# Kernel tuning notes

Measured on AMD Instinct MI355X. Metric: run time of the kernel, lower is better.

The kernel has to match this reference:

```python
import jax, jax.numpy as jnp
import numpy as np

EPS = 1e-8

def setup_inputs() -> dict:
    key = jax.random.key(0)
    ks = jax.random.split(key, 10)
    N, IN, Z, C, H = 8192, 512, 128, 64, 50
    x = jax.random.normal(ks[0], (N, IN), dtype=jnp.float32)
    c = jax.random.randint(ks[1], (N, 1), 0, C, dtype=jnp.int64)
    z = jax.random.normal(ks[2], (N, Z), dtype=jnp.float32)
    # f_x MLP params (Linear(IN,50) -> ReLU -> Linear(50,Z))
    W1 = jax.random.normal(ks[3], (IN, H), dtype=jnp.float32) / np.sqrt(IN)
    b1 = jax.random.normal(ks[4], (H,), dtype=jnp.float32) * 0.01
    W2 = jax.random.normal(ks[5], (H, Z), dtype=jnp.float32) / np.sqrt(H)
    b2 = jax.random.normal(ks[6], (Z,), dtype=jnp.float32) * 0.01
    # f_z Linear(Z,Z)
    Wz = jax.random.normal(ks[7], (Z, Z), dtype=jnp.float32) / np.sqrt(Z)
    bz = jax.random.normal(ks[8], (Z,), dtype=jnp.float32) * 0.01
    # per-category bilinear weights w_s [C,Z,Z] (torch.randn init)
    Ws = jax.random.normal(ks[9], (C, Z, Z), dtype=jnp.float32)
    return {"x": x, "c": c, "z": z, "W1": W1, "b1": b1, "W2": W2, "b2": b2, "Wz": Wz, "bz": bz, "Ws": Ws}

def reference(x, c, z, W1, b1, W2, b2, Wz, bz, Ws):
    cf = c.reshape(-1)                                    # [N]
    fx = jax.nn.relu(x @ W1 + b1) @ W2 + b2               # [N,Z]
    fz = z @ Wz + bz                                      # [N,Z]
    # per-sample bilinear: u[n] = fx[n] @ Ws[c[n]]
    u = jnp.einsum('nd,nde->ne', fx, Ws[cf])              # [N,Z]
    T = jax.nn.softplus(jnp.einsum('ne,ne->n', u, fz))    # [N]
    # neg_T[i] = mean over j with c[j]==c[i] of softplus(fx[i] @ Ws[c[i]] @ fz[j])
    S = jax.nn.softplus(u @ fz.T)                         # [N,N]
    mask = (cf[:, None] == cf[None, :]).astype(S.dtype)   # [N,N]
    neg_T = (S * mask).sum(axis=1) / mask.sum(axis=1)     # [N]
    return jnp.log(T + EPS) - jnp.log(neg_T + EPS)
```

## Files before the change

### kernel.cpp

```cpp
#include <hip/hip_runtime.h>
#include <math.h>

#define N_   8192
#define IN_  512
#define ZD   128
#define CC   64
#define HD   50
#define EPSF 1e-8f

typedef float vf4 __attribute__((ext_vector_type(4)));
typedef __attribute__((ext_vector_type(8))) short bfrag;

#define MFMA16(a, b, c) __builtin_amdgcn_mfma_f32_16x16x32_bf16((a), (b), (c), 0, 0, 0)

__device__ __forceinline__ float softplus_hot(float t) {
    return fmaxf(t, 0.f) + __logf(1.f + __expf(-fabsf(t)));
}
__device__ __forceinline__ float softplus_acc(float t) {
    return fmaxf(t, 0.f) + log1pf(expf(-fabsf(t)));
}
__device__ __forceinline__ unsigned short bf16_rn(float x) {
    unsigned int u = __float_as_uint(x);
    return (unsigned short)((u + 0x7fff + ((u >> 16) & 1)) >> 16);
}
__device__ __forceinline__ float bf16_f(unsigned short h) {
    return __uint_as_float(((unsigned int)h) << 16);
}
__device__ __forceinline__ void split8(const float* v, bfrag& hi, bfrag& lo) {
    #pragma unroll
    for (int e = 0; e < 8; ++e) {
        unsigned short h = bf16_rn(v[e]);
        ((short*)&hi)[e] = (short)h;
        ((short*)&lo)[e] = (short)bf16_rn(v[e] - bf16_f(h));
    }
}

__global__ __launch_bounds__(256) void k_pre(const int* __restrict__ c,
                                             const float* __restrict__ W1,
                                             const float* __restrict__ z,
                                             const float* __restrict__ Wz,
                                             const float* __restrict__ bz,
                                             const float* __restrict__ W2,
                                             const float* __restrict__ Ws,
                                             uint4* __restrict__ W1p,
                                             uint4* __restrict__ W2p,
                                             float* __restrict__ fz,
                                             unsigned short* __restrict__ fz_hi,
                                             unsigned short* __restrict__ Wst_hi,
                                             unsigned short* __restrict__ Wst_lo,
                                             int* __restrict__ counts,
                                             int* __restrict__ offsets,
                                             int* __restrict__ grouped) {
    __shared__ float smem[64 * 129];
    int tid = threadIdx.x;
    int b   = blockIdx.x;
    if (b < CC) {
        __shared__ int hist[CC];
        __shared__ int cursor;
        __shared__ int off_s;
        if (tid < CC) hist[tid] = 0;
        if (tid == 0) cursor = 0;
        __syncthreads();
        for (int i = tid; i < N_; i += 256) atomicAdd(&hist[c[i]], 1);
        __syncthreads();
        if (tid == 0) {
            int off = 0;
            for (int q = 0; q < b; ++q) off += hist[q];
            off_s = off;
            counts[b]  = hist[b];
            offsets[b] = off;
        }
        __syncthreads();
        int off = off_s;
        for (int i = tid; i < N_; i += 256) {
            if (c[i] == b) {
                int p = atomicAdd(&cursor, 1);
                grouped[off + p] = i;
            }
        }
    } else if (b < 80) {
        int unit = (b - 64) * 256 + tid;
        int lane = unit & 63, f = (unit >> 6) & 15, kc = unit >> 10;
        int nt = f >> 2, ks = f & 3;
        int n = nt * 16 + (lane & 15);
        int kbase = kc * 128 + ks * 32 + (lane >> 4) * 8;
        unsigned short hi8[8], lo8[8];
        #pragma unroll
        for (int j = 0; j < 8; ++j) {
            int k = kbase + j;
            float v = (n < HD) ? W1[k * HD + n] : 0.f;
            unsigned short h = bf16_rn(v);
            hi8[j] = h;
            lo8[j] = bf16_rn(v - bf16_f(h));
        }
        W1p[kc * 2048 + f * 64 + lane]        = *(uint4*)hi8;
        W1p[kc * 2048 + 1024 + f * 64 + lane] = *(uint4*)lo8;
    } else if (b < 84) {
        int unit = (b - 80) * 256 + tid;
        int lane = unit & 63, f = unit >> 6;
        int nt = f >> 1, ks = f & 1;
        int n = nt * 16 + (lane & 15);
        int kbase = ks * 32 + (lane >> 4) * 8;
        unsigned short hi8[8], lo8[8];
        #pragma unroll
        for (int j = 0; j < 8; ++j) {
            int k = kbase + j;
            float v = (k < HD) ? W2[k * ZD + n] : 0.f;
            unsigned short h = bf16_rn(v);
            hi8[j] = h;
            lo8[j] = bf16_rn(v - bf16_f(h));
        }
        W2p[f * 64 + lane]        = *(uint4*)hi8;
        W2p[1024 + f * 64 + lane] = *(uint4*)lo8;
    } else if (b < 212) {
        float* sz = smem;
        int row0 = (b - 84) * 64;
        vf4* s4 = (vf4*)sz;
        const vf4* z4 = (const vf4*)(z + (size_t)row0 * ZD);
        #pragma unroll
        for (int f = 0; f < 8; ++f) s4[tid + f * 256] = z4[tid + f * 256];
        __syncthreads();
        int cp = tid & 31, rgp = tid >> 5;
        const vf4* Wz4 = (const vf4*)Wz;
        vf4 bb = ((const vf4*)bz)[cp];
        vf4 acc[8];
        #pragma unroll
        for (int r = 0; r < 8; ++r) acc[r] = bb;
        #pragma unroll 1
        for (int d4 = 0; d4 < 32; ++d4) {
            vf4 w0 = Wz4[(4 * d4 + 0) * 32 + cp];
            vf4 w1 = Wz4[(4 * d4 + 1) * 32 + cp];
            vf4 w2 = Wz4[(4 * d4 + 2) * 32 + cp];
            vf4 w3 = Wz4[(4 * d4 + 3) * 32 + cp];
            #pragma unroll
            for (int r = 0; r < 8; ++r) {
                vf4 a = s4[(rgp * 8 + r) * 32 + d4];
                acc[r] += a[0] * w0;
                acc[r] += a[1] * w1;
                acc[r] += a[2] * w2;
                acc[r] += a[3] * w3;
            }
        }
        vf4* fz4 = (vf4*)fz;
        #pragma unroll
        for (int r = 0; r < 8; ++r) {
            int n = row0 + rgp * 8 + r;
            fz4[(size_t)n * 32 + cp] = acc[r];
            ushort4 h;
            h.x = bf16_rn(acc[r][0]); h.y = bf16_rn(acc[r][1]);
            h.z = bf16_rn(acc[r][2]); h.w = bf16_rn(acc[r][3]);
            *(ushort4*)(fz_hi + (size_t)n * ZD + cp * 4) = h;
        }
    } else {
        #pragma unroll 1
        for (int ci = 0; ci < 2; ++ci) {
            int cat = (b - 212) * 2 + ci;
            const float* Wc = Ws + (size_t)cat * ZD * ZD;
            unsigned short* Whi = Wst_hi + (size_t)cat * ZD * ZD;
            unsigned short* Wlo = Wst_lo + (size_t)cat * ZD * ZD;
            #pragma unroll 1
            for (int half = 0; half < 2; ++half) {
                __syncthreads();
                const vf4* src = (const vf4*)(Wc + (size_t)half * 64 * ZD);
                #pragma unroll
                for (int f = 0; f < 8; ++f) {
                    int idx = tid + f * 256;
                    int row = idx >> 5, q = idx & 31;
                    vf4 v = src[idx];
                    #pragma unroll
                    for (int e = 0; e < 4; ++e) smem[row * 129 + q * 4 + e] = v[e];
                }
                __syncthreads();
                #pragma unroll 1
                for (int f = 0; f < 32; ++f) {
                    int idx = tid + f * 256;
                    int e = idx >> 6, dd = idx & 63;
                    float v = smem[dd * 129 + e];
                    unsigned short h = bf16_rn(v);
                    Whi[(size_t)e * ZD + half * 64 + dd] = h;
                    Wlo[(size_t)e * ZD + half * 64 + dd] = bf16_rn(v - bf16_f(h));
                }
            }
        }
    }
}

__global__ __launch_bounds__(256) void k_hfx(const float* __restrict__ x,
                                             const uint4* __restrict__ W1p,
                                             const uint4* __restrict__ W2p,
                                             const float* __restrict__ b1,
                                             const float* __restrict__ b2,
                                             unsigned short* __restrict__ fx_hi,
                                             unsigned short* __restrict__ fx_lo) {
    __shared__ uint4 sW2[2048];
    __shared__ uint4 sW1[2048];
    __shared__ float sh[32 * 68];
    int tid = threadIdx.x;
    int lane = tid & 63, w = tid >> 6, m = lane & 15, quad = lane >> 4;
    int rg = w & 1, ch = w >> 1;
    int i0 = blockIdx.x * 32;

    #pragma unroll
    for (int f = 0; f < 8; ++f) sW2[tid + f * 256] = W2p[tid + f * 256];

    int row = i0 + rg * 16 + m;
    const float4* xr = (const float4*)(x + (size_t)row * IN_);

    vf4 accP[2], accQ[2];
    #pragma unroll
    for (int nt2 = 0; nt2 < 2; ++nt2) {
        accP[nt2] = (vf4){0.f, 0.f, 0.f, 0.f};
        accQ[nt2] = (vf4){0.f, 0.f, 0.f, 0.f};
    }

    #pragma unroll 1
    for (int kc = 0; kc < 4; ++kc) {
        __syncthreads();
        #pragma unroll
        for (int f = 0; f < 8; ++f)
            sW1[tid + f * 256] = W1p[kc * 2048 + tid + f * 256];
        __syncthreads();
        #pragma unroll 1
        for (int ks = 0; ks < 4; ++ks) {
            float4 xa = xr[kc * 32 + ks * 8 + quad * 2];
            float4 xb = xr[kc * 32 + ks * 8 + quad * 2 + 1];
            float xv[8] = {xa.x, xa.y, xa.z, xa.w, xb.x, xb.y, xb.z, xb.w};
            bfrag ah, al;
            split8(xv, ah, al);
            #pragma unroll
            for (int nt2 = 0; nt2 < 2; ++nt2) {
                int nt = ch * 2 + nt2;
                bfrag bh = *(const bfrag*)&sW1[(nt * 4 + ks) * 64 + lane];
                bfrag bl = *(const bfrag*)&sW1[1024 + (nt * 4 + ks) * 64 + lane];
                accP[nt2] = MFMA16(ah, bh, accP[nt2]);
                accQ[nt2] = MFMA16(ah, bl, accQ[nt2]);
                accQ[nt2] = MFMA16(al, bh, accQ[nt2]);
            }
        }
    }
    #pragma unroll
    for (int nt2 = 0; nt2 < 2; ++nt2) {
        int nt = ch * 2 + nt2;
        int col = nt * 16 + m;
        float bb = (col < HD) ? b1[col] : 0.f;
        vf4 acc = accP[nt2] + accQ[nt2];
        #pragma unroll
        for (int r = 0; r < 4; ++r)
            sh[(rg * 16 + quad * 4 + r) * 68 + col] = fmaxf(acc[r] + bb, 0.f);
    }
    __syncthreads();

    bfrag ah2[2], al2[2];
    #pragma unroll
    for (int ks = 0; ks < 2; ++ks) {
        const float4* shp = (const float4*)&sh[(rg * 16 + m) * 68 + ks * 32 + quad * 8];
        float4 ha = shp[0], hb = shp[1];
        float hv[8] = {ha.x, ha.y, ha.z, ha.w, hb.x, hb.y, hb.z, hb.w};
        split8(hv, ah2[ks], al2[ks]);
    }
    #pragma unroll 2
    for (int nt2 = 0; nt2 < 4; ++nt2) {
        int nt = ch * 4 + nt2;
        bfrag bh0 = *(const bfrag*)&sW2[(nt * 2 + 0) * 64 + lane];
        bfrag bl0 = *(const bfrag*)&sW2[1024 + (nt * 2 + 0) * 64 + lane];
        bfrag bh1 = *(const bfrag*)&sW2[(nt * 2 + 1) * 64 + lane];
        bfrag bl1 = *(const bfrag*)&sW2[1024 + (nt * 2 + 1) * 64 + lane];
        vf4 aA = {0.f, 0.f, 0.f, 0.f}, aB = {0.f, 0.f, 0.f, 0.f};
        aA = MFMA16(ah2[0], bh0, aA);
        aA = MFMA16(ah2[0], bl0, aA);
        aA = MFMA16(al2[0], bh0, aA);
        aB = MFMA16(ah2[1], bh1, aB);
        aB = MFMA16(ah2[1], bl1, aB);
        aB = MFMA16(al2[1], bh1, aB);
        vf4 a2 = aA + aB;
        int col = nt * 16 + m;
        float bb2 = b2[col];
        #pragma unroll
        for (int r = 0; r < 4; ++r) {
            size_t orow = (size_t)(i0 + rg * 16 + quad * 4 + r);
            float v = a2[r] + bb2;
            unsigned short hh = bf16_rn(v);
            fx_hi[orow * ZD + col] = hh;
            fx_lo[orow * ZD + col] = bf16_rn(v - bf16_f(hh));
        }
    }
}

#define TI 8
__global__ __launch_bounds__(256) void k_fused(const unsigned short* __restrict__ fx_hi,
                                               const unsigned short* __restrict__ fx_lo,
                                               const unsigned short* __restrict__ Wst_hi,
                                               const unsigned short* __restrict__ Wst_lo,
                                               const float* __restrict__ fz,
                                               const unsigned short* __restrict__ fz_hi,
                                               const int* __restrict__ grouped,
                                               const int* __restrict__ offsets,
                                               const int* __restrict__ counts,
                                               float* __restrict__ out) {
    __shared__ uint4 sWhi[128 * 17];
    __shared__ uint4 sWlo[128 * 17];
    __shared__ float sRed[2][2][16];
    int tid = threadIdx.x;
    int cat = blockIdx.x >> 3;
    int t   = blockIdx.x & (TI - 1);
    int off = offsets[cat], cnt = counts[cat];
    int i0 = t * 32;
    if (i0 >= cnt) return;
    int mI = min(32, cnt - i0);

    int lane = tid & 63, wave = tid >> 6;
    int m = lane & 15, quad = lane >> 4;
    int rg = wave & 1, eh = wave >> 1;

    const uint4* gh = (const uint4*)(Wst_hi + (size_t)cat * ZD * ZD);
    const uint4* gl = (const uint4*)(Wst_lo + (size_t)cat * ZD * ZD);
    #pragma unroll
    for (int f = 0; f < 8; ++f) {
        int idx = tid + f * 256;
        int e = idx >> 4, q = idx & 15;
        sWhi[e * 17 + q] = gh[idx];
        sWlo[e * 17 + q] = gl[idx];
    }

    int irow = rg * 16 + m;
    int n_gA = grouped[off + i0 + min(irow, mI - 1)];
    const unsigned short* fhp = fx_hi + (size_t)n_gA * ZD + quad * 8;
    const unsigned short* flp = fx_lo + (size_t)n_gA * ZD + quad * 8;
    bfrag a_hi[4], a_lo[4];
    #pragma unroll
    for (int kb = 0; kb < 4; ++kb) {
        a_hi[kb] = *(const bfrag*)(fhp + kb * 32);
        a_lo[kb] = *(const bfrag*)(flp + kb * 32);
    }
    __syncthreads();

    vf4 uacc[4];
    #pragma unroll 1
    for (int et2 = 0; et2 < 4; ++et2) {
        int et = eh * 4 + et2;
        vf4 aH = {0.f, 0.f, 0.f, 0.f};
        vf4 aM = {0.f, 0.f, 0.f, 0.f};
        vf4 aL = {0.f, 0.f, 0.f, 0.f};
        #pragma unroll
        for (int kb = 0; kb < 4; ++kb) {
            bfrag bh = *(const bfrag*)&sWhi[(et * 16 + m) * 17 + kb * 4 + quad];
            bfrag bl = *(const bfrag*)&sWlo[(et * 16 + m) * 17 + kb * 4 + quad];
            aH = MFMA16(a_hi[kb], bh, aH);
            aM = MFMA16(a_hi[kb], bl, aM);
            aL = MFMA16(a_lo[kb], bh, aL);
        }
        uacc[et2] = aH + aM + aL;
    }

    int nrow[4];
    #pragma unroll
    for (int r = 0; r < 4; ++r) {
        int ir = rg * 16 + quad * 4 + r;
        nrow[r] = (ir < mI) ? grouped[off + i0 + ir] : -1;
    }
    float fzv[4][4];
    #pragma unroll
    for (int et2 = 0; et2 < 4; ++et2) {
        #pragma unroll
        for (int r = 0; r < 4; ++r) {
            fzv[et2][r] = 0.f;
            if (nrow[r] >= 0)
                fzv[et2][r] = fz[(size_t)nrow[r] * ZD + (eh * 4 + et2) * 16 + m];
        }
    }
    float p[4] = {0.f, 0.f, 0.f, 0.f};
    #pragma unroll
    for (int et2 = 0; et2 < 4; ++et2) {
        #pragma unroll
        for (int r = 0; r < 4; ++r) p[r] += uacc[et2][r] * fzv[et2][r];
    }
    #pragma unroll
    for (int r = 0; r < 4; ++r) {
        float v = p[r];
        #pragma unroll
        for (int s = 8; s >= 1; s >>= 1) v += __shfl_xor(v, s, 64);
        p[r] = v;
    }
    if (m == 0) {
        #pragma unroll
        for (int r = 0; r < 4; ++r) sRed[rg][eh][quad * 4 + r] = p[r];
    }
    __syncthreads();

    unsigned short* su = (unsigned short*)sWhi;
    #pragma unroll
    for (int et2 = 0; et2 < 4; ++et2) {
        int col = (eh * 4 + et2) * 16 + m;
        #pragma unroll
        for (int r = 0; r < 4; ++r)
            su[(rg * 16 + quad * 4 + r) * 136 + col] = bf16_rn(uacc[et2][r]);
    }
    float logT_r[4] = {0.f, 0.f, 0.f, 0.f};
    if (eh == 0) {
        #pragma unroll
        for (int r = 0; r < 4; ++r) {
            float pt = sRed[rg][0][quad * 4 + r] + sRed[rg][1][quad * 4 + r];
            logT_r[r] = logf(softplus_acc(pt) + EPSF);
        }
    }
    __syncthreads();

    bfrag na[4];
    #pragma unroll
    for (int kb = 0; kb < 4; ++kb)
        na[kb] = *(const bfrag*)&su[(rg * 16 + m) * 136 + kb * 32 + quad * 8];

    uint4* sB = (uint4*)sWlo;
    float negsum[4] = {0.f, 0.f, 0.f, 0.f};

    #pragma unroll 1
    for (int jb = 0; jb < cnt; jb += 64) {
        int mJ = min(64, cnt - jb);
        __syncthreads();
        #pragma unroll
        for (int f = 0; f < 4; ++f) {
            int idx = tid + f * 256;
            int jr = idx >> 4, q = idx & 15;
            uint4 v = {0u, 0u, 0u, 0u};
            if (jr < mJ) {
                int j_g = grouped[off + jb + jr];
                v = *(const uint4*)(fz_hi + (size_t)j_g * ZD + q * 8);
            }
            sB[jr * 17 + q] = v;
        }
        __syncthreads();
        #pragma unroll
        for (int jt2 = 0; jt2 < 2; ++jt2) {
            int jt = eh * 2 + jt2;
            bfrag b0 = *(const bfrag*)&sB[(jt * 16 + m) * 17 + 0 + quad];
            bfrag b1 = *(const bfrag*)&sB[(jt * 16 + m) * 17 + 4 + quad];
            bfrag b2 = *(const bfrag*)&sB[(jt * 16 + m) * 17 + 8 + quad];
            bfrag b3 = *(const bfrag*)&sB[(jt * 16 + m) * 17 + 12 + quad];
            vf4 aA = {0.f, 0.f, 0.f, 0.f}, aB = {0.f, 0.f, 0.f, 0.f};
            aA = MFMA16(na[0], b0, aA);
            aA = MFMA16(na[1], b1, aA);
            aB = MFMA16(na[2], b2, aB);
            aB = MFMA16(na[3], b3, aB);
            vf4 acc = aA + aB;
            bool jok = (jt * 16 + m) < mJ;
            #pragma unroll
            for (int r = 0; r < 4; ++r)
                if (jok) negsum[r] += softplus_hot(acc[r]);
        }
    }

    #pragma unroll
    for (int r = 0; r < 4; ++r) {
        float v = negsum[r];
        #pragma unroll
        for (int s = 8; s >= 1; s >>= 1) v += __shfl_xor(v, s, 64);
        negsum[r] = v;
    }
    if (m == 0) {
        #pragma unroll
        for (int r = 0; r < 4; ++r) sRed[rg][eh][quad * 4 + r] = negsum[r];
    }
    __syncthreads();
    if (eh == 0 && m == 0) {
        #pragma unroll
        for (int r = 0; r < 4; ++r) {
            if (nrow[r] >= 0) {
                float tot = sRed[rg][0][quad * 4 + r] + sRed[rg][1][quad * 4 + r];
                out[nrow[r]] = logT_r[r] - logf(tot / (float)cnt + EPSF);
            }
        }
    }
}

extern "C" void kernel_launch(void* const* d_in, const int* in_sizes, int n_in,
                              void* d_out, int out_size, void* d_ws, size_t ws_size,
                              hipStream_t stream) {
    const float* x  = (const float*)d_in[0];
    const int*   c  = (const int*)  d_in[1];
    const float* z  = (const float*)d_in[2];
    const float* W1 = (const float*)d_in[3];
    const float* b1 = (const float*)d_in[4];
    const float* W2 = (const float*)d_in[5];
    const float* b2 = (const float*)d_in[6];
    const float* Wz = (const float*)d_in[7];
    const float* bz = (const float*)d_in[8];
    const float* Ws = (const float*)d_in[9];
    float* out = (float*)d_out;

    uint4* W1p = (uint4*)d_ws;
    uint4* W2p = W1p + 8192;
    float* fz  = (float*)(W2p + 2048);
    unsigned short* fx_hi  = (unsigned short*)(fz + (size_t)N_ * ZD);
    unsigned short* fx_lo  = fx_hi + (size_t)N_ * ZD;
    unsigned short* fz_hi  = fx_lo + (size_t)N_ * ZD;
    unsigned short* Wst_hi = fz_hi + (size_t)N_ * ZD;
    unsigned short* Wst_lo = Wst_hi + (size_t)CC * ZD * ZD;
    int* counts  = (int*)(Wst_lo + (size_t)CC * ZD * ZD);
    int* offsets = counts + CC;
    int* grouped = offsets + CC;

    k_pre   <<<244, 256, 0, stream>>>(c, W1, z, Wz, bz, W2, Ws, W1p, W2p, fz,
                                      fz_hi, Wst_hi, Wst_lo, counts, offsets,
                                      grouped);
    k_hfx   <<<N_ / 32, 256, 0, stream>>>(x, W1p, W2p, b1, b2, fx_hi, fx_lo);
    k_fused <<<CC * TI, 256, 0, stream>>>(fx_hi, fx_lo, Wst_hi, Wst_lo, fz,
                                          fz_hi, grouped, offsets, counts, out);
}
```

Measured before the change: 131.7 us.

## Double block size to 512 threads and halve per-wave tile work

Both k_hfx and k_fused now launch 512-thread blocks (8 waves instead of 4). Each wave covers half as many output column tiles, and cross-wave reductions are widened to four partial sums. The goal is more waves in flight to hide memory and MFMA latency on small per-category tiles. The cost is more block-level synchronisation, shared reductions across more waves, and duplicated A-fragment loads per wave.

After: 131.2 us. Within noise of the previous version (-0.4%).

```diff
diff --git a/kernel.cpp b/kernel.cpp
--- a/kernel.cpp
+++ b/kernel.cpp
@@ -185,7 +185,7 @@
     }
 }
 
-__global__ __launch_bounds__(256) void k_hfx(const float* __restrict__ x,
+__global__ __launch_bounds__(512) void k_hfx(const float* __restrict__ x,
                                              const uint4* __restrict__ W1p,
                                              const uint4* __restrict__ W2p,
                                              const float* __restrict__ b1,
@@ -201,24 +201,21 @@
     int i0 = blockIdx.x * 32;
 
     #pragma unroll
-    for (int f = 0; f < 8; ++f) sW2[tid + f * 256] = W2p[tid + f * 256];
+    for (int f = 0; f < 4; ++f) sW2[tid + f * 512] = W2p[tid + f * 512];
 
     int row = i0 + rg * 16 + m;
     const float4* xr = (const float4*)(x + (size_t)row * IN_);
 
-    vf4 accP[2], accQ[2];
-    #pragma unroll
-    for (int nt2 = 0; nt2 < 2; ++nt2) {
-        accP[nt2] = (vf4){0.f, 0.f, 0.f, 0.f};
-        accQ[nt2] = (vf4){0.f, 0.f, 0.f, 0.f};
-    }
+    vf4 accP = {0.f, 0.f, 0.f, 0.f};
+    vf4 accQ = {0.f, 0.f, 0.f, 0.f};
+    vf4 accR = {0.f, 0.f, 0.f, 0.f};
 
     #pragma unroll 1
     for (int kc = 0; kc < 4; ++kc) {
         __syncthreads();
         #pragma unroll
-        for (int f = 0; f < 8; ++f)
-            sW1[tid + f * 256] = W1p[kc * 2048 + tid + f * 256];
+        for (int f = 0; f < 4; ++f)
+            sW1[tid + f * 512] = W1p[kc * 2048 + tid + f * 512];
         __syncthreads();
         #pragma unroll 1
         for (int ks = 0; ks < 4; ++ks) {
@@ -227,23 +224,17 @@
             float xv[8] = {xa.x, xa.y, xa.z, xa.w, xb.x, xb.y, xb.z, xb.w};
             bfrag ah, al;
             split8(xv, ah, al);
-            #pragma unroll
-            for (int nt2 = 0; nt2 < 2; ++nt2) {
-                int nt = ch * 2 + nt2;
-                bfrag bh = *(const bfrag*)&sW1[(nt * 4 + ks) * 64 + lane];
-                bfrag bl = *(const bfrag*)&sW1[1024 + (nt * 4 + ks) * 64 + lane];
-                accP[nt2] = MFMA16(ah, bh, accP[nt2]);
-                accQ[nt2] = MFMA16(ah, bl, accQ[nt2]);
-                accQ[nt2] = MFMA16(al, bh, accQ[nt2]);
-            }
-        }
-    }
-    #pragma unroll
-    for (int nt2 = 0; nt2 < 2; ++nt2) {
-        int nt = ch * 2 + nt2;
-        int col = nt * 16 + m;
+            bfrag bh = *(const bfrag*)&sW1[(ch * 4 + ks) * 64 + lane];
+            bfrag bl = *(const bfrag*)&sW1[1024 + (ch * 4 + ks) * 64 + lane];
+            accP = MFMA16(ah, bh, accP);
+            accQ = MFMA16(ah, bl, accQ);
+            accR = MFMA16(al, bh, accR);
+        }
+    }
+    {
+        int col = ch * 16 + m;
         float bb = (col < HD) ? b1[col] : 0.f;
-        vf4 acc = accP[nt2] + accQ[nt2];
+        vf4 acc = accP + accQ + accR;
         #pragma unroll
         for (int r = 0; r < 4; ++r)
             sh[(rg * 16 + quad * 4 + r) * 68 + col] = fmaxf(acc[r] + bb, 0.f);
@@ -258,9 +249,9 @@
         float hv[8] = {ha.x, ha.y, ha.z, ha.w, hb.x, hb.y, hb.z, hb.w};
         split8(hv, ah2[ks], al2[ks]);
     }
-    #pragma unroll 2
-    for (int nt2 = 0; nt2 < 4; ++nt2) {
-        int nt = ch * 4 + nt2;
+    #pragma unroll
+    for (int nt2 = 0; nt2 < 2; ++nt2) {
+        int nt = ch * 2 + nt2;
         bfrag bh0 = *(const bfrag*)&sW2[(nt * 2 + 0) * 64 + lane];
         bfrag bl0 = *(const bfrag*)&sW2[1024 + (nt * 2 + 0) * 64 + lane];
         bfrag bh1 = *(const bfrag*)&sW2[(nt * 2 + 1) * 64 + lane];
@@ -287,7 +278,7 @@
 }
 
 #define TI 8
-__global__ __launch_bounds__(256) void k_fused(const unsigned short* __restrict__ fx_hi,
+__global__ __launch_bounds__(512) void k_fused(const unsigned short* __restrict__ fx_hi,
                                                const unsigned short* __restrict__ fx_lo,
                                                const unsigned short* __restrict__ Wst_hi,
                                                const unsigned short* __restrict__ Wst_lo,
@@ -299,7 +290,7 @@
                                                float* __restrict__ out) {
     __shared__ uint4 sWhi[128 * 17];
     __shared__ uint4 sWlo[128 * 17];
-    __shared__ float sRed[2][2][16];
+    __shared__ float sRed[2][4][16];
     int tid = threadIdx.x;
     int cat = blockIdx.x >> 3;
     int t   = blockIdx.x & (TI - 1);
@@ -315,8 +306,8 @@
     const uint4* gh = (const uint4*)(Wst_hi + (size_t)cat * ZD * ZD);
     const uint4* gl = (const uint4*)(Wst_lo + (size_t)cat * ZD * ZD);
     #pragma unroll
-    for (int f = 0; f < 8; ++f) {
-        int idx = tid + f * 256;
+    for (int f = 0; f < 4; ++f) {
+        int idx = tid + f * 512;
         int e = idx >> 4, q = idx & 15;
         sWhi[e * 17 + q] = gh[idx];
         sWlo[e * 17 + q] = gl[idx];
@@ -334,10 +325,10 @@
     }
     __syncthreads();
 
-    vf4 uacc[4];
+    vf4 uacc[2];
     #pragma unroll 1
-    for (int et2 = 0; et2 < 4; ++et2) {
-        int et = eh * 4 + et2;
+    for (int et2 = 0; et2 < 2; ++et2) {
+        int et = eh * 2 + et2;
         vf4 aH = {0.f, 0.f, 0.f, 0.f};
         vf4 aM = {0.f, 0.f, 0.f, 0.f};
         vf4 aL = {0.f, 0.f, 0.f, 0.f};
@@ -358,19 +349,19 @@
         int ir = rg * 16 + quad * 4 + r;
         nrow[r] = (ir < mI) ? grouped[off + i0 + ir] : -1;
     }
-    float fzv[4][4];
-    #pragma unroll
-    for (int et2 = 0; et2 < 4; ++et2) {
+    float fzv[2][4];
+    #pragma unroll
+    for (int et2 = 0; et2 < 2; ++et2) {
         #pragma unroll
         for (int r = 0; r < 4; ++r) {
             fzv[et2][r] = 0.f;
             if (nrow[r] >= 0)
-                fzv[et2][r] = fz[(size_t)nrow[r] * ZD + (eh * 4 + et2) * 16 + m];
+                fzv[et2][r] = fz[(size_t)nrow[r] * ZD + (eh * 2 + et2) * 16 + m];
         }
     }
     float p[4] = {0.f, 0.f, 0.f, 0.f};
     #pragma unroll
-    for (int et2 = 0; et2 < 4; ++et2) {
+    for (int et2 = 0; et2 < 2; ++et2) {
         #pragma unroll
         for (int r = 0; r < 4; ++r) p[r] += uacc[et2][r] * fzv[et2][r];
     }
@@ -389,8 +380,8 @@
 
     unsigned short* su = (unsigned short*)sWhi;
     #pragma unroll
-    for (int et2 = 0; et2 < 4; ++et2) {
-        int col = (eh * 4 + et2) * 16 + m;
+    for (int et2 = 0; et2 < 2; ++et2) {
+        int col = (eh * 2 + et2) * 16 + m;
         #pragma unroll
         for (int r = 0; r < 4; ++r)
             su[(rg * 16 + quad * 4 + r) * 136 + col] = bf16_rn(uacc[et2][r]);
@@ -399,7 +390,8 @@
     if (eh == 0) {
         #pragma unroll
         for (int r = 0; r < 4; ++r) {
-            float pt = sRed[rg][0][quad * 4 + r] + sRed[rg][1][quad * 4 + r];
+            float pt = sRed[rg][0][quad * 4 + r] + sRed[rg][1][quad * 4 + r]
+                     + sRed[rg][2][quad * 4 + r] + sRed[rg][3][quad * 4 + r];
             logT_r[r] = logf(softplus_acc(pt) + EPSF);
         }
     }
@@ -418,8 +410,8 @@
         int mJ = min(64, cnt - jb);
         __syncthreads();
         #pragma unroll
-        for (int f = 0; f < 4; ++f) {
-            int idx = tid + f * 256;
+        for (int f = 0; f < 2; ++f) {
+            int idx = tid + f * 512;
             int jr = idx >> 4, q = idx & 15;
             uint4 v = {0u, 0u, 0u, 0u};
             if (jr < mJ) {
@@ -429,9 +421,8 @@
             sB[jr * 17 + q] = v;
         }
         __syncthreads();
-        #pragma unroll
-        for (int jt2 = 0; jt2 < 2; ++jt2) {
-            int jt = eh * 2 + jt2;
+        {
+            int jt = eh;
             bfrag b0 = *(const bfrag*)&sB[(jt * 16 + m) * 17 + 0 + quad];
             bfrag b1 = *(const bfrag*)&sB[(jt * 16 + m) * 17 + 4 + quad];
             bfrag b2 = *(const bfrag*)&sB[(jt * 16 + m) * 17 + 8 + quad];
@@ -465,7 +456,8 @@
         #pragma unroll
         for (int r = 0; r < 4; ++r) {
             if (nrow[r] >= 0) {
-                float tot = sRed[rg][0][quad * 4 + r] + sRed[rg][1][quad * 4 + r];
+                float tot = sRed[rg][0][quad * 4 + r] + sRed[rg][1][quad * 4 + r]
+                          + sRed[rg][2][quad * 4 + r] + sRed[rg][3][quad * 4 + r];
                 out[nrow[r]] = logT_r[r] - logf(tot / (float)cnt + EPSF);
             }
         }
@@ -502,7 +494,7 @@
     k_pre   <<<244, 256, 0, stream>>>(c, W1, z, Wz, bz, W2, Ws, W1p, W2p, fz,
                                       fz_hi, Wst_hi, Wst_lo, counts, offsets,
                                       grouped);
-    k_hfx   <<<N_ / 32, 256, 0, stream>>>(x, W1p, W2p, b1, b2, fx_hi, fx_lo);
-    k_fused <<<CC * TI, 256, 0, stream>>>(fx_hi, fx_lo, Wst_hi, Wst_lo, fz,
+    k_hfx   <<<N_ / 32, 512, 0, stream>>>(x, W1p, W2p, b1, b2, fx_hi, fx_lo);
+    k_fused <<<CC * TI, 512, 0, stream>>>(fx_hi, fx_lo, Wst_hi, Wst_lo, fz,
                                           fz_hi, grouped, offsets, counts, out);
 }
```
